# Optimization experiments

Measured on AMD Instinct MI355X. Metric: run time of the kernel, lower is better.

## Reference

```python
import jax, jax.numpy as jnp
import numpy as np

N = 100000
E = 1600000
F_IN = 256
H1, C1 = 8, 8          # conv1: 8 heads x 8 channels -> 64
H2, C2 = 1, 32         # conv2: 1 head x num_classes
SLOPE = 0.2


def gat_conv(x, src, dst, n, W, a_src, a_dst, b, heads, out):
    # x: [n, f_in]; W: [f_in, heads*out]; a_src/a_dst: [heads, out]; b: [heads*out]
    h = (x @ W).reshape(n, heads, out)                       # [n, H, C]
    s = jnp.sum(h * a_src, axis=-1)                          # [n, H]
    d = jnp.sum(h * a_dst, axis=-1)                          # [n, H]
    e = jax.nn.leaky_relu(s[src] + d[dst], SLOPE)            # [e, H]
    m = jax.ops.segment_max(e, dst, num_segments=n)          # stable segment softmax
    ex = jnp.exp(e - m[dst])
    z = jax.ops.segment_sum(ex, dst, num_segments=n)
    alpha = ex / (z[dst] + 1e-16)                            # [e, H]
    msg = alpha[:, :, None] * h[src]                         # [e, H, C]
    agg = jax.ops.segment_sum(msg, dst, num_segments=n)      # [n, H, C]
    return agg.reshape(n, heads * out) + b


def setup_inputs() -> dict:
    key = jax.random.key(0)
    ks = jax.random.split(key, 10)
    x = jax.random.normal(ks[0], (N, F_IN), dtype=jnp.float32)
    edge_index = jax.random.randint(ks[1], (2, E), 0, N, dtype=jnp.int32)
    sc = 0.05
    W1 = jax.random.normal(ks[2], (F_IN, H1 * C1), dtype=jnp.float32) * sc
    att_src1 = jax.random.normal(ks[3], (H1, C1), dtype=jnp.float32) * sc
    att_dst1 = jax.random.normal(ks[4], (H1, C1), dtype=jnp.float32) * sc
    b1 = jnp.zeros((H1 * C1,), dtype=jnp.float32)
    W2 = jax.random.normal(ks[5], (H1 * C1, H2 * C2), dtype=jnp.float32) * sc
    att_src2 = jax.random.normal(ks[6], (H2, C2), dtype=jnp.float32) * sc
    att_dst2 = jax.random.normal(ks[7], (H2, C2), dtype=jnp.float32) * sc
    b2 = jnp.zeros((H2 * C2,), dtype=jnp.float32)
    return {"x": x, "edge_index": edge_index, "W1": W1, "att_src1": att_src1,
            "att_dst1": att_dst1, "b1": b1, "W2": W2, "att_src2": att_src2,
            "att_dst2": att_dst2, "b2": b2}


def reference(x, edge_index, W1, att_src1, att_dst1, b1, W2, att_src2, att_dst2, b2):
    # add self loops (PyG GATConv default)
    loops = jnp.arange(N, dtype=edge_index.dtype)
    src = jnp.concatenate([edge_index[0], loops])
    dst = jnp.concatenate([edge_index[1], loops])
    # dropout layers are identity in eval mode
    h = gat_conv(x, src, dst, N, W1, att_src1, att_dst1, b1, H1, C1)
    h = jax.nn.elu(h)
    h = gat_conv(h, src, dst, N, W2, att_src2, att_dst2, b2, H2, C2)
    return jax.nn.log_softmax(h, axis=1)
```

## Files before the change

### kernel.cpp

```cpp
#include <hip/hip_runtime.h>
#include <hip/hip_bf16.h>

#define N_NODES 100000
#define N_EDGES 1600000
#define N_TOT   (N_EDGES + N_NODES)
#define F_IN    256
#define F1      64
#define H1      8
#define C1      8
#define F2      32
#define SLOPE   0.2f

#define NB_G    ((N_NODES + 255) / 256)

#define EB      4096
#define NB1     ((N_EDGES + EB - 1) / EB)
#define BW      256
#define NBKT    ((N_NODES + BW - 1) / BW)

typedef unsigned int  uint;
typedef unsigned short ushort;
typedef __attribute__((ext_vector_type(8))) short bf16x8;
typedef __attribute__((ext_vector_type(4))) float f32x4;
typedef __attribute__((ext_vector_type(2))) float f32x2;

__device__ inline ushort f2bf(float f) {
    uint u = __float_as_uint(f);
    uint r = u + 0x7fffu + ((u >> 16) & 1u);
    return (ushort)(r >> 16);
}
__device__ inline float bflo(uint u) { return __uint_as_float(u << 16); }
__device__ inline float bfhi(uint u) { return __uint_as_float(u & 0xffff0000u); }
__device__ inline uint pk2bf(float a, float b) {
    __hip_bfloat162 h = __float22bfloat162_rn(make_float2(a, b));
    union { __hip_bfloat162 h; uint u; } cv; cv.h = h;
    return cv.u;
}

__device__ inline void bucket_bases(const int* __restrict__ colsum,
                                    int* sc, int* sb, int tid) {
    const int i0 = 2 * tid, i1 = 2 * tid + 1;
    const int a0 = (i0 < NBKT) ? colsum[i0] : 0;
    const int a1 = (i1 < NBKT) ? colsum[i1] : 0;
    sc[tid] = a0 + a1;
    __syncthreads();
    for (int off = 1; off < 256; off <<= 1) {
        int t = (tid >= off) ? sc[tid - off] : 0;
        __syncthreads();
        sc[tid] += t;
        __syncthreads();
    }
    const int excl = sc[tid] - (a0 + a1);
    if (i0 < NBKT)  sb[i0] = excl;
    if (i1 <= NBKT) sb[i1] = excl + a0;
    __syncthreads();
}

__global__ __launch_bounds__(256) void k_gemm1_p1(
        const float* __restrict__ x, const float* __restrict__ W1,
        const float* __restrict__ as1, const float* __restrict__ ad1,
        const int* __restrict__ ei,
        uint* __restrict__ sh1, float* __restrict__ d1,
        int* __restrict__ bcnt) {
    __shared__ union {
        ushort B[F_IN * F1];
        ushort S[4][64][66];
        int    H[NBKT];
    } sm;
    const int tid = threadIdx.x;

    if (blockIdx.x >= NB_G) {
        const int blk = blockIdx.x - NB_G;
        for (int j = tid; j < NBKT; j += 256) sm.H[j] = 0;
        __syncthreads();
        const int e0 = blk * EB;
        const int lim = (e0 + EB < N_EDGES) ? e0 + EB : N_EDGES;
        for (int i = e0 + tid; i < lim; i += 256)
            atomicAdd(&sm.H[ei[N_EDGES + i] >> 8], 1);
        __syncthreads();
        for (int j = tid; j < NBKT; j += 256)
            bcnt[j * NB1 + blk] = sm.H[j];
        return;
    }

    for (int i = 0; i < 64; ++i) {
        const int e = i * 256 + tid;
        const int k = e >> 6, n = e & 63;
        sm.B[((k >> 3) * 64 + n) * 8 + (k & 7)] = f2bf(W1[e]);
    }
    __syncthreads();

    const int wave = tid >> 6, lane = tid & 63;
    const int q = lane >> 4, ln = lane & 15;
    const int rowbase = blockIdx.x * 256 + wave * 64;

    f32x4 acc[4][4];
#pragma unroll
    for (int mt = 0; mt < 4; ++mt)
#pragma unroll
        for (int nt = 0; nt < 4; ++nt) acc[mt][nt] = (f32x4){0.f, 0.f, 0.f, 0.f};

    int rows[4];
#pragma unroll
    for (int mt = 0; mt < 4; ++mt) {
        const int r = rowbase + mt * 16 + ln;
        rows[mt] = r < N_NODES ? r : N_NODES - 1;
    }

    for (int t = 0; t < 8; ++t) {
        bf16x8 bfr[4];
#pragma unroll
        for (int nt = 0; nt < 4; ++nt)
            bfr[nt] = *(const bf16x8*)&sm.B[((t * 4 + q) * 64 + nt * 16 + ln) * 8];
#pragma unroll
        for (int mt = 0; mt < 4; ++mt) {
            const float4* ap = (const float4*)(x + (size_t)rows[mt] * F_IN + t * 32 + q * 8);
            const float4 a0 = ap[0], a1 = ap[1];
            uint4 au = make_uint4(pk2bf(a0.x, a0.y), pk2bf(a0.z, a0.w),
                                  pk2bf(a1.x, a1.y), pk2bf(a1.z, a1.w));
            bf16x8 af = *(bf16x8*)&au;
#pragma unroll
            for (int nt = 0; nt < 4; ++nt)
                acc[mt][nt] = __builtin_amdgcn_mfma_f32_16x16x32_bf16(
                                  af, bfr[nt], acc[mt][nt], 0, 0, 0);
        }
    }
    __syncthreads();

#pragma unroll
    for (int mt = 0; mt < 4; ++mt)
#pragma unroll
        for (int nt = 0; nt < 4; ++nt)
#pragma unroll
            for (int r = 0; r < 4; ++r)
                sm.S[wave][mt * 16 + q * 4 + r][nt * 16 + ln] = f2bf(acc[mt][nt][r]);
    __syncthreads();

    const int node = rowbase + lane;
    if (node >= N_NODES) return;
    const uint* srow = (const uint*)&sm.S[wave][lane][0];
    float sacc[H1], dacc[H1];
#pragma unroll
    for (int h = 0; h < H1; ++h) { sacc[h] = 0.f; dacc[h] = 0.f; }
    uint* rowp = sh1 + (size_t)node * 40;
#pragma unroll
    for (int p4 = 0; p4 < 8; ++p4) {
        const uint u0 = srow[p4 * 4 + 0], u1 = srow[p4 * 4 + 1];
        const uint u2 = srow[p4 * 4 + 2], u3 = srow[p4 * 4 + 3];
        ((uint4*)rowp)[2 + p4] = make_uint4(u0, u1, u2, u3);
        const float c[8] = {bflo(u0), bfhi(u0), bflo(u1), bfhi(u1),
                            bflo(u2), bfhi(u2), bflo(u3), bfhi(u3)};
#pragma unroll
        for (int j = 0; j < 8; ++j) {
            sacc[p4] += c[j] * as1[p4 * 8 + j];
            dacc[p4] += c[j] * ad1[p4 * 8 + j];
        }
    }
    ((float4*)rowp)[0] = make_float4(sacc[0], sacc[1], sacc[2], sacc[3]);
    ((float4*)rowp)[1] = make_float4(sacc[4], sacc[5], sacc[6], sacc[7]);
    float4* d4 = (float4*)(d1 + (size_t)node * H1);
    d4[0] = make_float4(dacc[0], dacc[1], dacc[2], dacc[3]);
    d4[1] = make_float4(dacc[4], dacc[5], dacc[6], dacc[7]);
}

__global__ __launch_bounds__(64) void k_p2(
        int* __restrict__ bcnt, int* __restrict__ colsum) {
    const int col = blockIdx.x, lane = threadIdx.x;
    int carry = 0;
    for (int c0 = 0; c0 < NB1; c0 += 64) {
        const int idx = c0 + lane;
        const int v = (idx < NB1) ? bcnt[col * NB1 + idx] : 0;
        int s = v;
#pragma unroll
        for (int off = 1; off < 64; off <<= 1) {
            int u = __shfl_up(s, off);
            if (lane >= off) s += u;
        }
        if (idx < NB1) bcnt[col * NB1 + idx] = carry + s - v;
        carry += __shfl(s, 63);
    }
    if (lane == 0) colsum[col] = carry;
}

__global__ __launch_bounds__(256) void k_p3(
        const int* __restrict__ ei, const int* __restrict__ bcnt,
        const int* __restrict__ colsum, uint* __restrict__ tmp) {
    __shared__ int sc[256];
    __shared__ int cur[NBKT + 1];
    const int tid = threadIdx.x, blk = blockIdx.x;
    bucket_bases(colsum, sc, cur, tid);
    for (int b = tid; b < NBKT; b += 256) cur[b] += bcnt[b * NB1 + blk];
    __syncthreads();
    const int e0 = blk * EB;
    const int lim = (e0 + EB < N_EDGES) ? e0 + EB : N_EDGES;
    for (int i = e0 + tid; i < lim; i += 256) {
        const int s = ei[i], d = ei[N_EDGES + i];
        const int pos = atomicAdd(&cur[d >> 8], 1);
        tmp[pos] = ((uint)(d & 255) << 24) | (uint)s;
    }
}

__global__ __launch_bounds__(256) void k_final(
        const uint* __restrict__ tmp, const int* __restrict__ colsum,
        int* __restrict__ row_ptr, int* __restrict__ srcs) {
    __shared__ int sc[256];
    __shared__ int sb[NBKT + 1];
    __shared__ int cur[BW];
    const int tid = threadIdx.x, b = blockIdx.x;
    bucket_bases(colsum, sc, sb, tid);
    cur[tid] = 0;
    __syncthreads();
    const int lo = sb[b], hi = sb[b + 1];
    for (int i = lo + tid; i < hi; i += 256)
        atomicAdd(&cur[tmp[i] >> 24], 1);
    __syncthreads();
    const int n = b * BW + tid;
    const int myc = cur[tid];
    const int v = (n < N_NODES) ? myc + 1 : 0;
    sc[tid] = v;
    __syncthreads();
    for (int off = 1; off < 256; off <<= 1) {
        int t = (tid >= off) ? sc[tid - off] : 0;
        __syncthreads();
        sc[tid] += t;
        __syncthreads();
    }
    const int rp = sb[b] + b * BW + (sc[tid] - v);
    if (n < N_NODES) {
        row_ptr[n] = rp;
        srcs[rp] = n;
    }
    if (b == NBKT - 1 && tid == 255) row_ptr[N_NODES] = N_TOT;
    cur[tid] = rp + 1;
    __syncthreads();
    for (int i = lo + tid; i < hi; i += 256) {
        const uint u = tmp[i];
        const int pos = atomicAdd(&cur[u >> 24], 1);
        srcs[pos] = (int)(u & 0xFFFFFFu);
    }
}

__global__ __launch_bounds__(256) void k_agg1(
        const int* __restrict__ row_ptr, const int* __restrict__ srcs,
        const uint* __restrict__ sh1, const float* __restrict__ d1,
        const float* __restrict__ b1,
        const float* __restrict__ W2, const float* __restrict__ as2,
        const float* __restrict__ ad2,
        ushort* __restrict__ h2b, float* __restrict__ s2,
        float* __restrict__ d2) {
    __shared__ float sx[4][64];
    const int wid = (blockIdx.x * 256 + threadIdx.x) >> 6;
    if (wid >= N_NODES) return;
    const int w = threadIdx.x >> 6;
    const int lane = threadIdx.x & 63;
    const int q = lane >> 3;
    const int c = lane & 7;
    const int so = 4 * c;
    const int ho = 32 + 16 * c;
    const float dh = d1[(size_t)wid * H1 + c];
    const int beg = row_ptr[wid], end = row_ptr[wid + 1];
    const char* base = (const char*)sh1;
    f32x2 A0 = {0.f, 0.f}, A1 = {0.f, 0.f}, A2 = {0.f, 0.f}, A3 = {0.f, 0.f};
    float z = 0.f;
    int i = beg + q;
    for (; i + 8 < end; i += 16) {
        const int sA = srcs[i], sB = srcs[i + 8];
        const char* rA = base + (size_t)sA * 160;
        const char* rB = base + (size_t)sB * 160;
        float eA = *(const float*)(rA + so) + dh;
        float eB = *(const float*)(rB + so) + dh;
        eA = fmaxf(eA, SLOPE * eA);
        eB = fmaxf(eB, SLOPE * eB);
        const float xA = __expf(eA), xB = __expf(eB);
        const uint4 UA = *(const uint4*)(rA + ho);
        const uint4 UB = *(const uint4*)(rB + ho);
        z += xA + xB;
        const f32x2 xa = {xA, xA}, xb = {xB, xB};
        A0 += xa * (f32x2){bflo(UA.x), bfhi(UA.x)};
        A1 += xa * (f32x2){bflo(UA.y), bfhi(UA.y)};
        A2 += xa * (f32x2){bflo(UA.z), bfhi(UA.z)};
        A3 += xa * (f32x2){bflo(UA.w), bfhi(UA.w)};
        A0 += xb * (f32x2){bflo(UB.x), bfhi(UB.x)};
        A1 += xb * (f32x2){bflo(UB.y), bfhi(UB.y)};
        A2 += xb * (f32x2){bflo(UB.z), bfhi(UB.z)};
        A3 += xb * (f32x2){bflo(UB.w), bfhi(UB.w)};
    }
    for (; i < end; i += 8) {
        const int sA = srcs[i];
        const char* rA = base + (size_t)sA * 160;
        float eA = *(const float*)(rA + so) + dh;
        eA = fmaxf(eA, SLOPE * eA);
        const float xA = __expf(eA);
        const uint4 UA = *(const uint4*)(rA + ho);
        z += xA;
        const f32x2 xa = {xA, xA};
        A0 += xa * (f32x2){bflo(UA.x), bfhi(UA.x)};
        A1 += xa * (f32x2){bflo(UA.y), bfhi(UA.y)};
        A2 += xa * (f32x2){bflo(UA.z), bfhi(UA.z)};
        A3 += xa * (f32x2){bflo(UA.w), bfhi(UA.w)};
    }
    f32x2 r0, r1;
    {
        const bool hi = lane & 8;
        f32x2 snd0 = hi ? A0 : A2, snd1 = hi ? A1 : A3;
        const f32x2 kp0 = hi ? A2 : A0, kp1 = hi ? A3 : A1;
        snd0.x = __shfl_xor(snd0.x, 8); snd0.y = __shfl_xor(snd0.y, 8);
        snd1.x = __shfl_xor(snd1.x, 8); snd1.y = __shfl_xor(snd1.y, 8);
        r0 = kp0 + snd0; r1 = kp1 + snd1;
    }
    {
        const bool hi = lane & 16;
        f32x2 snd = hi ? r0 : r1;
        const f32x2 kp = hi ? r1 : r0;
        snd.x = __shfl_xor(snd.x, 16); snd.y = __shfl_xor(snd.y, 16);
        r0 = kp + snd;
    }
    float sv;
    {
        const bool hi = lane & 32;
        float snd = hi ? r0.x : r0.y;
        const float kp = hi ? r0.y : r0.x;
        snd = __shfl_xor(snd, 32);
        sv = kp + snd;
    }
    z += __shfl_xor(z, 8); z += __shfl_xor(z, 16); z += __shfl_xor(z, 32);

    const int j = (((lane >> 3) & 1) << 2) | (((lane >> 4) & 1) << 1)
                | ((lane >> 5) & 1);
    const int xi = c * 8 + j;
    const float zi = 1.f / (z + 1e-16f);
    float xv = sv * zi + b1[xi];
    xv = xv > 0.f ? xv : __expf(xv) - 1.f;
    sx[w][xi] = xv;
    __builtin_amdgcn_wave_barrier();

    const int kh = lane >> 5;
    const int oc = lane & 31;
    const float4* sxv = (const float4*)&sx[w][kh * 32];
    const float* wp0 = W2 + (size_t)(kh * 32) * F2 + oc;
    float acc = 0.f;
#pragma unroll
    for (int k4 = 0; k4 < 8; ++k4) {
        const float4 xv4 = sxv[k4];
        const float* wp = wp0 + (size_t)k4 * 4 * F2;
        acc += xv4.x * wp[0]      + xv4.y * wp[F2]
             + xv4.z * wp[2 * F2] + xv4.w * wp[3 * F2];
    }
    acc += __shfl_xor(acc, 32);

    float sA2 = acc * as2[oc], dA2 = acc * ad2[oc];
#pragma unroll
    for (int off = 1; off <= 16; off <<= 1) {
        sA2 += __shfl_xor(sA2, off);
        dA2 += __shfl_xor(dA2, off);
    }
    const float accp = __shfl_xor(acc, 1);
    if (lane < 32 && !(lane & 1))
        *(uint*)&h2b[(size_t)wid * F2 + oc] = pk2bf(acc, accp);
    if (lane == 0) { s2[wid] = sA2; d2[wid] = dA2; }
}

__global__ __launch_bounds__(256) void k_agg2(
        const int* __restrict__ row_ptr, const int* __restrict__ srcs,
        const ushort* __restrict__ h2b, const float* __restrict__ s2,
        const float* __restrict__ d2, const float* __restrict__ b2,
        float* __restrict__ out) {
    const int wid = (blockIdx.x * 256 + threadIdx.x) >> 6;
    if (wid >= N_NODES) return;
    const int lane = threadIdx.x & 63;
    const int q = lane >> 2;
    const int c = lane & 3;
    const float dn = d2[wid];
    const int beg = row_ptr[wid], end = row_ptr[wid + 1];
    const uint4* hv = (const uint4*)h2b;
    f32x2 A0 = {0.f, 0.f}, A1 = {0.f, 0.f}, A2 = {0.f, 0.f}, A3 = {0.f, 0.f};
    float z = 0.f;
    int i = beg + q;
    for (; i + 16 < end; i += 32) {
        const int sA = srcs[i], sB = srcs[i + 16];
        float eA = s2[sA] + dn;
        float eB = s2[sB] + dn;
        eA = fmaxf(eA, SLOPE * eA);
        eB = fmaxf(eB, SLOPE * eB);
        const float xA = __expf(eA), xB = __expf(eB);
        const uint4 UA = hv[(size_t)sA * 4 + c];
        const uint4 UB = hv[(size_t)sB * 4 + c];
        z += xA + xB;
        const f32x2 xa = {xA, xA}, xb = {xB, xB};
        A0 += xa * (f32x2){bflo(UA.x), bfhi(UA.x)};
        A1 += xa * (f32x2){bflo(UA.y), bfhi(UA.y)};
        A2 += xa * (f32x2){bflo(UA.z), bfhi(UA.z)};
        A3 += xa * (f32x2){bflo(UA.w), bfhi(UA.w)};
        A0 += xb * (f32x2){bflo(UB.x), bfhi(UB.x)};
        A1 += xb * (f32x2){bflo(UB.y), bfhi(UB.y)};
        A2 += xb * (f32x2){bflo(UB.z), bfhi(UB.z)};
        A3 += xb * (f32x2){bflo(UB.w), bfhi(UB.w)};
    }
    for (; i < end; i += 16) {
        const int sA = srcs[i];
        float eA = s2[sA] + dn;
        eA = fmaxf(eA, SLOPE * eA);
        const float xA = __expf(eA);
        const uint4 UA = hv[(size_t)sA * 4 + c];
        z += xA;
        const f32x2 xa = {xA, xA};
        A0 += xa * (f32x2){bflo(UA.x), bfhi(UA.x)};
        A1 += xa * (f32x2){bflo(UA.y), bfhi(UA.y)};
        A2 += xa * (f32x2){bflo(UA.z), bfhi(UA.z)};
        A3 += xa * (f32x2){bflo(UA.w), bfhi(UA.w)};
    }
    f32x2 r0, r1;
    {
        const bool hi = lane & 4;
        f32x2 snd0 = hi ? A0 : A2, snd1 = hi ? A1 : A3;
        const f32x2 kp0 = hi ? A2 : A0, kp1 = hi ? A3 : A1;
        snd0.x = __shfl_xor(snd0.x, 4); snd0.y = __shfl_xor(snd0.y, 4);
        snd1.x = __shfl_xor(snd1.x, 4); snd1.y = __shfl_xor(snd1.y, 4);
        r0 = kp0 + snd0; r1 = kp1 + snd1;
    }
    {
        const bool hi = lane & 8;
        f32x2 snd = hi ? r0 : r1;
        const f32x2 kp = hi ? r1 : r0;
        snd.x = __shfl_xor(snd.x, 8); snd.y = __shfl_xor(snd.y, 8);
        r0 = kp + snd;
    }
    float sv;
    {
        const bool hi = lane & 16;
        float snd = hi ? r0.x : r0.y;
        const float kp = hi ? r0.y : r0.x;
        snd = __shfl_xor(snd, 16);
        sv = kp + snd;
    }
    sv += __shfl_xor(sv, 32);
    z += __shfl_xor(z, 4); z += __shfl_xor(z, 8);
    z += __shfl_xor(z, 16); z += __shfl_xor(z, 32);

    const int j = (((lane >> 2) & 1) << 2) | (((lane >> 3) & 1) << 1)
                | ((lane >> 4) & 1);
    const int elem = c * 8 + j;
    const float zi = 1.f / (z + 1e-16f);
    const float v = sv * zi + b2[elem];
    float m = v;
#pragma unroll
    for (int off = 1; off <= 16; off <<= 1) m = fmaxf(m, __shfl_xor(m, off));
    float ssum = __expf(v - m);
#pragma unroll
    for (int off = 1; off <= 16; off <<= 1) ssum += __shfl_xor(ssum, off);
    const float lse = m + __logf(ssum);
    if (lane < 32) out[(size_t)wid * F2 + elem] = v - lse;
}

extern "C" void kernel_launch(void* const* d_in, const int* in_sizes, int n_in,
                              void* d_out, int out_size, void* d_ws, size_t ws_size,
                              hipStream_t stream) {
    const float* x   = (const float*)d_in[0];
    const int*   ei  = (const int*)d_in[1];
    const float* W1  = (const float*)d_in[2];
    const float* as1 = (const float*)d_in[3];
    const float* ad1 = (const float*)d_in[4];
    const float* b1  = (const float*)d_in[5];
    const float* W2  = (const float*)d_in[6];
    const float* as2 = (const float*)d_in[7];
    const float* ad2 = (const float*)d_in[8];
    const float* b2  = (const float*)d_in[9];
    float* out = (float*)d_out;

    uint*   sh1 = (uint*)d_ws;
    ushort* h2b = (ushort*)(sh1 + (size_t)N_NODES * 40);
    float*  d1  = (float*)(h2b + (size_t)N_NODES * F2);
    float*  s2  = d1 + (size_t)N_NODES * H1;
    float*  d2  = s2 + N_NODES;
    uint*   tmp = (uint*)(d2 + N_NODES);
    int* row_ptr = (int*)(tmp + N_EDGES);
    int* colsum  = row_ptr + N_NODES + 1;
    int* bcnt    = colsum + NBKT;
    int* srcs    = bcnt + (size_t)NBKT * NB1;

    const int nb_w = (N_NODES * 64 + 255) / 256;

    k_gemm1_p1<<<NB_G + NB1, 256, 0, stream>>>(x, W1, as1, ad1, ei,
                                               sh1, d1, bcnt);
    k_p2<<<NBKT, 64, 0, stream>>>(bcnt, colsum);
    k_p3<<<NB1, 256, 0, stream>>>(ei, bcnt, colsum, tmp);
    k_final<<<NBKT, 256, 0, stream>>>(tmp, colsum, row_ptr, srcs);
    k_agg1<<<nb_w, 256, 0, stream>>>(row_ptr, srcs, sh1, d1, b1,
                                     W2, as2, ad2, h2b, s2, d2);
    k_agg2<<<nb_w, 256, 0, stream>>>(row_ptr, srcs, h2b, s2, d2, b2, out);
}
```

Baseline: 342.2 us.

## Move GEMM1 into final CSR kernel and split h1 into separate arrays

The layer-1 GEMM moves out of the first histogram kernel and runs as extra blocks in the final CSR-build kernel. W1 is converted to bf16 once by a dedicated block in the histogram kernel and loaded into LDS with vector copies. The fused 160-byte row (scores plus features) is split into a 128-byte bf16 feature array and separate s1/d1 float arrays, so aggregation gathers aligned feature rows and small score rows separately. This aims to balance the GEMM against the light CSR kernels and tidy the gather layout, at the cost of two separate gathers per edge in agg1.

```diff
diff --git a/kernel.cpp b/kernel.cpp
--- a/kernel.cpp
+++ b/kernel.cpp
@@ -56,111 +56,29 @@
     __syncthreads();
 }
 
-__global__ __launch_bounds__(256) void k_gemm1_p1(
-        const float* __restrict__ x, const float* __restrict__ W1,
-        const float* __restrict__ as1, const float* __restrict__ ad1,
-        const int* __restrict__ ei,
-        uint* __restrict__ sh1, float* __restrict__ d1,
-        int* __restrict__ bcnt) {
-    __shared__ union {
-        ushort B[F_IN * F1];
-        ushort S[4][64][66];
-        int    H[NBKT];
-    } sm;
+__global__ __launch_bounds__(256) void k_p1w(
+        const int* __restrict__ ei, const float* __restrict__ W1,
+        int* __restrict__ bcnt, ushort* __restrict__ w1b) {
+    __shared__ int H[NBKT];
     const int tid = threadIdx.x;
-
-    if (blockIdx.x >= NB_G) {
-        const int blk = blockIdx.x - NB_G;
-        for (int j = tid; j < NBKT; j += 256) sm.H[j] = 0;
-        __syncthreads();
-        const int e0 = blk * EB;
-        const int lim = (e0 + EB < N_EDGES) ? e0 + EB : N_EDGES;
-        for (int i = e0 + tid; i < lim; i += 256)
-            atomicAdd(&sm.H[ei[N_EDGES + i] >> 8], 1);
-        __syncthreads();
-        for (int j = tid; j < NBKT; j += 256)
-            bcnt[j * NB1 + blk] = sm.H[j];
+    if (blockIdx.x == NB1) {
+        for (int i = 0; i < 64; ++i) {
+            const int e = i * 256 + tid;
+            const int k = e >> 6, n = e & 63;
+            w1b[((k >> 3) * 64 + n) * 8 + (k & 7)] = f2bf(W1[e]);
+        }
         return;
     }
-
-    for (int i = 0; i < 64; ++i) {
-        const int e = i * 256 + tid;
-        const int k = e >> 6, n = e & 63;
-        sm.B[((k >> 3) * 64 + n) * 8 + (k & 7)] = f2bf(W1[e]);
-    }
-    __syncthreads();
-
-    const int wave = tid >> 6, lane = tid & 63;
-    const int q = lane >> 4, ln = lane & 15;
-    const int rowbase = blockIdx.x * 256 + wave * 64;
-
-    f32x4 acc[4][4];
-#pragma unroll
-    for (int mt = 0; mt < 4; ++mt)
-#pragma unroll
-        for (int nt = 0; nt < 4; ++nt) acc[mt][nt] = (f32x4){0.f, 0.f, 0.f, 0.f};
-
-    int rows[4];
-#pragma unroll
-    for (int mt = 0; mt < 4; ++mt) {
-        const int r = rowbase + mt * 16 + ln;
-        rows[mt] = r < N_NODES ? r : N_NODES - 1;
-    }
-
-    for (int t = 0; t < 8; ++t) {
-        bf16x8 bfr[4];
-#pragma unroll
-        for (int nt = 0; nt < 4; ++nt)
-            bfr[nt] = *(const bf16x8*)&sm.B[((t * 4 + q) * 64 + nt * 16 + ln) * 8];
-#pragma unroll
-        for (int mt = 0; mt < 4; ++mt) {
-            const float4* ap = (const float4*)(x + (size_t)rows[mt] * F_IN + t * 32 + q * 8);
-            const float4 a0 = ap[0], a1 = ap[1];
-            uint4 au = make_uint4(pk2bf(a0.x, a0.y), pk2bf(a0.z, a0.w),
-                                  pk2bf(a1.x, a1.y), pk2bf(a1.z, a1.w));
-            bf16x8 af = *(bf16x8*)&au;
-#pragma unroll
-            for (int nt = 0; nt < 4; ++nt)
-                acc[mt][nt] = __builtin_amdgcn_mfma_f32_16x16x32_bf16(
-                                  af, bfr[nt], acc[mt][nt], 0, 0, 0);
-        }
-    }
-    __syncthreads();
-
-#pragma unroll
-    for (int mt = 0; mt < 4; ++mt)
-#pragma unroll
-        for (int nt = 0; nt < 4; ++nt)
-#pragma unroll
-            for (int r = 0; r < 4; ++r)
-                sm.S[wave][mt * 16 + q * 4 + r][nt * 16 + ln] = f2bf(acc[mt][nt][r]);
-    __syncthreads();
-
-    const int node = rowbase + lane;
-    if (node >= N_NODES) return;
-    const uint* srow = (const uint*)&sm.S[wave][lane][0];
-    float sacc[H1], dacc[H1];
-#pragma unroll
-    for (int h = 0; h < H1; ++h) { sacc[h] = 0.f; dacc[h] = 0.f; }
-    uint* rowp = sh1 + (size_t)node * 40;
-#pragma unroll
-    for (int p4 = 0; p4 < 8; ++p4) {
-        const uint u0 = srow[p4 * 4 + 0], u1 = srow[p4 * 4 + 1];
-        const uint u2 = srow[p4 * 4 + 2], u3 = srow[p4 * 4 + 3];
-        ((uint4*)rowp)[2 + p4] = make_uint4(u0, u1, u2, u3);
-        const float c[8] = {bflo(u0), bfhi(u0), bflo(u1), bfhi(u1),
-                            bflo(u2), bfhi(u2), bflo(u3), bfhi(u3)};
-#pragma unroll
-        for (int j = 0; j < 8; ++j) {
-            sacc[p4] += c[j] * as1[p4 * 8 + j];
-            dacc[p4] += c[j] * ad1[p4 * 8 + j];
-        }
-    }
-    ((float4*)rowp)[0] = make_float4(sacc[0], sacc[1], sacc[2], sacc[3]);
-    ((float4*)rowp)[1] = make_float4(sacc[4], sacc[5], sacc[6], sacc[7]);
-    float4* d4 = (float4*)(d1 + (size_t)node * H1);
-    d4[0] = make_float4(dacc[0], dacc[1], dacc[2], dacc[3]);
-    d4[1] = make_float4(dacc[4], dacc[5], dacc[6], dacc[7]);
+    const int blk = blockIdx.x;
+    for (int j = tid; j < NBKT; j += 256) H[j] = 0;
+    __syncthreads();
+    const int e0 = blk * EB;
+    const int lim = (e0 + EB < N_EDGES) ? e0 + EB : N_EDGES;
+    for (int i = e0 + tid; i < lim; i += 256)
+        atomicAdd(&H[ei[N_EDGES + i] >> 8], 1);
+    __syncthreads();
+    for (int j = tid; j < NBKT; j += 256)
+        bcnt[j * NB1 + blk] = H[j];
 }
 
 __global__ __launch_bounds__(64) void k_p2(
@@ -200,50 +118,144 @@
     }
 }
 
-__global__ __launch_bounds__(256) void k_final(
+__global__ __launch_bounds__(256) void k_final_gemm(
         const uint* __restrict__ tmp, const int* __restrict__ colsum,
-        int* __restrict__ row_ptr, int* __restrict__ srcs) {
-    __shared__ int sc[256];
-    __shared__ int sb[NBKT + 1];
-    __shared__ int cur[BW];
-    const int tid = threadIdx.x, b = blockIdx.x;
-    bucket_bases(colsum, sc, sb, tid);
-    cur[tid] = 0;
-    __syncthreads();
-    const int lo = sb[b], hi = sb[b + 1];
-    for (int i = lo + tid; i < hi; i += 256)
-        atomicAdd(&cur[tmp[i] >> 24], 1);
-    __syncthreads();
-    const int n = b * BW + tid;
-    const int myc = cur[tid];
-    const int v = (n < N_NODES) ? myc + 1 : 0;
-    sc[tid] = v;
-    __syncthreads();
-    for (int off = 1; off < 256; off <<= 1) {
-        int t = (tid >= off) ? sc[tid - off] : 0;
-        __syncthreads();
-        sc[tid] += t;
-        __syncthreads();
-    }
-    const int rp = sb[b] + b * BW + (sc[tid] - v);
-    if (n < N_NODES) {
-        row_ptr[n] = rp;
-        srcs[rp] = n;
-    }
-    if (b == NBKT - 1 && tid == 255) row_ptr[N_NODES] = N_TOT;
-    cur[tid] = rp + 1;
-    __syncthreads();
-    for (int i = lo + tid; i < hi; i += 256) {
-        const uint u = tmp[i];
-        const int pos = atomicAdd(&cur[u >> 24], 1);
-        srcs[pos] = (int)(u & 0xFFFFFFu);
-    }
+        int* __restrict__ row_ptr, int* __restrict__ srcs,
+        const float* __restrict__ x, const ushort* __restrict__ w1b,
+        const float* __restrict__ as1, const float* __restrict__ ad1,
+        ushort* __restrict__ h1b, float* __restrict__ s1,
+        float* __restrict__ d1) {
+    __shared__ union {
+        struct { int sc[256]; int sb[NBKT + 1]; int cur[BW]; } f;
+        ushort B[F_IN * F1];
+        ushort S[4][64][66];
+    } sm;
+    const int tid = threadIdx.x;
+
+    if (blockIdx.x < NBKT) {
+        const int b = blockIdx.x;
+        bucket_bases(colsum, sm.f.sc, sm.f.sb, tid);
+        sm.f.cur[tid] = 0;
+        __syncthreads();
+        const int lo = sm.f.sb[b], hi = sm.f.sb[b + 1];
+        for (int i = lo + tid; i < hi; i += 256)
+            atomicAdd(&sm.f.cur[tmp[i] >> 24], 1);
+        __syncthreads();
+        const int n = b * BW + tid;
+        const int myc = sm.f.cur[tid];
+        const int v = (n < N_NODES) ? myc + 1 : 0;
+        __syncthreads();
+        sm.f.sc[tid] = v;
+        __syncthreads();
+        for (int off = 1; off < 256; off <<= 1) {
+            int t = (tid >= off) ? sm.f.sc[tid - off] : 0;
+            __syncthreads();
+            sm.f.sc[tid] += t;
+            __syncthreads();
+        }
+        const int rp = lo + b * BW + (sm.f.sc[tid] - v);
+        if (n < N_NODES) {
+            row_ptr[n] = rp;
+            srcs[rp] = n;
+        }
+        if (b == NBKT - 1 && tid == 255) row_ptr[N_NODES] = N_TOT;
+        sm.f.cur[tid] = rp + 1;
+        __syncthreads();
+        for (int i = lo + tid; i < hi; i += 256) {
+            const uint u = tmp[i];
+            const int pos = atomicAdd(&sm.f.cur[u >> 24], 1);
+            srcs[pos] = (int)(u & 0xFFFFFFu);
+        }
+        return;
+    }
+
+    {
+        const uint4* s4 = (const uint4*)w1b;
+        uint4* d4 = (uint4*)sm.B;
+#pragma unroll
+        for (int i = 0; i < 8; ++i)
+            d4[i * 256 + tid] = s4[i * 256 + tid];
+    }
+    __syncthreads();
+
+    const int wave = tid >> 6, lane = tid & 63;
+    const int q = lane >> 4, ln = lane & 15;
+    const int rowbase = (blockIdx.x - NBKT) * 256 + wave * 64;
+
+    f32x4 acc[4][4];
+#pragma unroll
+    for (int mt = 0; mt < 4; ++mt)
+#pragma unroll
+        for (int nt = 0; nt < 4; ++nt) acc[mt][nt] = (f32x4){0.f, 0.f, 0.f, 0.f};
+
+    int rows[4];
+#pragma unroll
+    for (int mt = 0; mt < 4; ++mt) {
+        const int r = rowbase + mt * 16 + ln;
+        rows[mt] = r < N_NODES ? r : N_NODES - 1;
+    }
+
+    for (int t = 0; t < 8; ++t) {
+        bf16x8 bfr[4];
+#pragma unroll
+        for (int nt = 0; nt < 4; ++nt)
+            bfr[nt] = *(const bf16x8*)&sm.B[((t * 4 + q) * 64 + nt * 16 + ln) * 8];
+#pragma unroll
+        for (int mt = 0; mt < 4; ++mt) {
+            const float4* ap = (const float4*)(x + (size_t)rows[mt] * F_IN + t * 32 + q * 8);
+            const float4 a0 = ap[0], a1 = ap[1];
+            uint4 au = make_uint4(pk2bf(a0.x, a0.y), pk2bf(a0.z, a0.w),
+                                  pk2bf(a1.x, a1.y), pk2bf(a1.z, a1.w));
+            bf16x8 af = *(bf16x8*)&au;
+#pragma unroll
+            for (int nt = 0; nt < 4; ++nt)
+                acc[mt][nt] = __builtin_amdgcn_mfma_f32_16x16x32_bf16(
+                                  af, bfr[nt], acc[mt][nt], 0, 0, 0);
+        }
+    }
+    __syncthreads();
+
+#pragma unroll
+    for (int mt = 0; mt < 4; ++mt)
+#pragma unroll
+        for (int nt = 0; nt < 4; ++nt)
+#pragma unroll
+            for (int r = 0; r < 4; ++r)
+                sm.S[wave][mt * 16 + q * 4 + r][nt * 16 + ln] = f2bf(acc[mt][nt][r]);
+    __syncthreads();
+
+    const int node = rowbase + lane;
+    if (node >= N_NODES) return;
+    const uint* srow = (const uint*)&sm.S[wave][lane][0];
+    float sacc[H1], dacc[H1];
+#pragma unroll
+    for (int h = 0; h < H1; ++h) { sacc[h] = 0.f; dacc[h] = 0.f; }
+    uint4* hout = (uint4*)(h1b + (size_t)node * F1);
+#pragma unroll
+    for (int p4 = 0; p4 < 8; ++p4) {
+        const uint u0 = srow[p4 * 4 + 0], u1 = srow[p4 * 4 + 1];
+        const uint u2 = srow[p4 * 4 + 2], u3 = srow[p4 * 4 + 3];
+        hout[p4] = make_uint4(u0, u1, u2, u3);
+        const float c[8] = {bflo(u0), bfhi(u0), bflo(u1), bfhi(u1),
+                            bflo(u2), bfhi(u2), bflo(u3), bfhi(u3)};
+#pragma unroll
+        for (int j = 0; j < 8; ++j) {
+            sacc[p4] += c[j] * as1[p4 * 8 + j];
+            dacc[p4] += c[j] * ad1[p4 * 8 + j];
+        }
+    }
+    float4* s4 = (float4*)(s1 + (size_t)node * H1);
+    float4* d4 = (float4*)(d1 + (size_t)node * H1);
+    s4[0] = make_float4(sacc[0], sacc[1], sacc[2], sacc[3]);
+    s4[1] = make_float4(sacc[4], sacc[5], sacc[6], sacc[7]);
+    d4[0] = make_float4(dacc[0], dacc[1], dacc[2], dacc[3]);
+    d4[1] = make_float4(dacc[4], dacc[5], dacc[6], dacc[7]);
 }
 
 __global__ __launch_bounds__(256) void k_agg1(
         const int* __restrict__ row_ptr, const int* __restrict__ srcs,
-        const uint* __restrict__ sh1, const float* __restrict__ d1,
-        const float* __restrict__ b1,
+        const ushort* __restrict__ h1b, const float* __restrict__ s1,
+        const float* __restrict__ d1, const float* __restrict__ b1,
         const float* __restrict__ W2, const float* __restrict__ as2,
         const float* __restrict__ ad2,
         ushort* __restrict__ h2b, float* __restrict__ s2,
@@ -255,25 +267,21 @@
     const int lane = threadIdx.x & 63;
     const int q = lane >> 3;
     const int c = lane & 7;
-    const int so = 4 * c;
-    const int ho = 32 + 16 * c;
     const float dh = d1[(size_t)wid * H1 + c];
     const int beg = row_ptr[wid], end = row_ptr[wid + 1];
-    const char* base = (const char*)sh1;
+    const uint4* hv = (const uint4*)h1b;
     f32x2 A0 = {0.f, 0.f}, A1 = {0.f, 0.f}, A2 = {0.f, 0.f}, A3 = {0.f, 0.f};
     float z = 0.f;
     int i = beg + q;
     for (; i + 8 < end; i += 16) {
         const int sA = srcs[i], sB = srcs[i + 8];
-        const char* rA = base + (size_t)sA * 160;
-        const char* rB = base + (size_t)sB * 160;
-        float eA = *(const float*)(rA + so) + dh;
-        float eB = *(const float*)(rB + so) + dh;
+        float eA = s1[(size_t)sA * H1 + c] + dh;
+        float eB = s1[(size_t)sB * H1 + c] + dh;
         eA = fmaxf(eA, SLOPE * eA);
         eB = fmaxf(eB, SLOPE * eB);
         const float xA = __expf(eA), xB = __expf(eB);
-        const uint4 UA = *(const uint4*)(rA + ho);
-        const uint4 UB = *(const uint4*)(rB + ho);
+        const uint4 UA = hv[(size_t)sA * 8 + c];
+        const uint4 UB = hv[(size_t)sB * 8 + c];
         z += xA + xB;
         const f32x2 xa = {xA, xA}, xb = {xB, xB};
         A0 += xa * (f32x2){bflo(UA.x), bfhi(UA.x)};
@@ -287,11 +295,10 @@
     }
     for (; i < end; i += 8) {
         const int sA = srcs[i];
-        const char* rA = base + (size_t)sA * 160;
-        float eA = *(const float*)(rA + so) + dh;
+        float eA = s1[(size_t)sA * H1 + c] + dh;
         eA = fmaxf(eA, SLOPE * eA);
         const float xA = __expf(eA);
-        const uint4 UA = *(const uint4*)(rA + ho);
+        const uint4 UA = hv[(size_t)sA * 8 + c];
         z += xA;
         const f32x2 xa = {xA, xA};
         A0 += xa * (f32x2){bflo(UA.x), bfhi(UA.x)};
@@ -467,9 +474,11 @@
     const float* b2  = (const float*)d_in[9];
     float* out = (float*)d_out;
 
-    uint*   sh1 = (uint*)d_ws;
-    ushort* h2b = (ushort*)(sh1 + (size_t)N_NODES * 40);
-    float*  d1  = (float*)(h2b + (size_t)N_NODES * F2);
+    ushort* h1b = (ushort*)d_ws;
+    ushort* h2b = h1b + (size_t)N_NODES * F1;
+    ushort* w1b = h2b + (size_t)N_NODES * F2;
+    float*  s1  = (float*)(w1b + F_IN * F1);
+    float*  d1  = s1 + (size_t)N_NODES * H1;
     float*  s2  = d1 + (size_t)N_NODES * H1;
     float*  d2  = s2 + N_NODES;
     uint*   tmp = (uint*)(d2 + N_NODES);
@@ -480,12 +489,13 @@
 
     const int nb_w = (N_NODES * 64 + 255) / 256;
 
-    k_gemm1_p1<<<NB_G + NB1, 256, 0, stream>>>(x, W1, as1, ad1, ei,
-                                               sh1, d1, bcnt);
+    k_p1w<<<NB1 + 1, 256, 0, stream>>>(ei, W1, bcnt, w1b);
     k_p2<<<NBKT, 64, 0, stream>>>(bcnt, colsum);
     k_p3<<<NB1, 256, 0, stream>>>(ei, bcnt, colsum, tmp);
-    k_final<<<NBKT, 256, 0, stream>>>(tmp, colsum, row_ptr, srcs);
-    k_agg1<<<nb_w, 256, 0, stream>>>(row_ptr, srcs, sh1, d1, b1,
+    k_final_gemm<<<NBKT + NB_G, 256, 0, stream>>>(tmp, colsum, row_ptr, srcs,
+                                                  x, w1b, as1, ad1,
+                                                  h1b, s1, d1);
+    k_agg1<<<nb_w, 256, 0, stream>>>(row_ptr, srcs, h1b, s1, d1, b1,
                                      W2, as2, ad2, h2b, s2, d2);
     k_agg2<<<nb_w, 256, 0, stream>>>(row_ptr, srcs, h2b, s2, d2, b2, out);
 }
```

Result: slower. 354.3 us (+3.6%).
